# Optimization experiments

Measured on AMD Instinct MI355X. Metric: run time of the kernel, lower is better.

## Reference

```python
import jax, jax.numpy as jnp
import numpy as np


def _sample_choices(prob_weights, key):
    # softmax over edge-type dim, take P(NORMAL_EDGE)=index 1
    prob_edge = jax.nn.softmax(prob_weights, axis=-1)[..., 1]  # [out, in]
    k_bern, k_fix = jax.random.split(key)
    choices = jax.random.bernoulli(k_bern, prob_edge).astype(prob_weights.dtype)  # [out, in]
    # zero-connection fixup: rows with no sampled edge get one random connection
    out_f, in_f = choices.shape
    conn_count = jnp.sum(choices, axis=-1)  # [out]
    rand_cols = jax.random.randint(k_fix, (out_f,), 0, in_f)  # [out]
    fix = ((conn_count == 0)[:, None] & (jnp.arange(in_f)[None, :] == rand_cols[:, None]))
    choices = choices + fix.astype(choices.dtype)
    # selected edges -> 0, unselected -> 1 (min operator branch; no *-1 negation)
    mask = jnp.abs(choices - 1.0)
    return mask


def reference(x, prob_weights):
    # x: [B, in], prob_weights: [out, in, 2]
    mask = _sample_choices(prob_weights, jax.random.key(42))  # [out, in]
    # result[b, o] = min_i (x[b, i] + mask[o, i])  -- [B, out, in] intermediate
    operator_inputs = x[:, None, :] + mask[None, :, :]
    return jnp.min(operator_inputs, axis=-1)  # [B, out]


def setup_inputs() -> dict:
    key = jax.random.key(0)
    k_x, k_w = jax.random.split(key)
    B, IN, OUT = 512, 512, 512
    x = jax.random.uniform(k_x, (B, IN), dtype=jnp.float32)
    prob_weights = jax.random.uniform(k_w, (OUT, IN, 2), dtype=jnp.float32)
    return {"x": x, "prob_weights": prob_weights}
```

## Files before the change

### kernel.cpp

```cpp
#include <hip/hip_runtime.h>
#include <cstdint>

__host__ __device__ inline void threefry2x32(uint32_t k0, uint32_t k1,
                                             uint32_t x0, uint32_t x1,
                                             uint32_t& o0, uint32_t& o1) {
  const uint32_t ks2 = k0 ^ k1 ^ 0x1BD11BDAu;
  uint32_t v0 = x0 + k0, v1 = x1 + k1;
#define RL(v, r) (((v) << (r)) | ((v) >> (32 - (r))))
#define RND4(a, b, c, d)                                                       \
  v0 += v1; v1 = RL(v1, a); v1 ^= v0;                                          \
  v0 += v1; v1 = RL(v1, b); v1 ^= v0;                                          \
  v0 += v1; v1 = RL(v1, c); v1 ^= v0;                                          \
  v0 += v1; v1 = RL(v1, d); v1 ^= v0;
  RND4(13, 15, 26, 6)  v0 += k1;  v1 += ks2 + 1u;
  RND4(17, 29, 16, 24) v0 += ks2; v1 += k0 + 2u;
  RND4(13, 15, 26, 6)  v0 += k0;  v1 += k1 + 3u;
  RND4(17, 29, 16, 24) v0 += k1;  v1 += ks2 + 4u;
  RND4(13, 15, 26, 6)  v0 += ks2; v1 += k0 + 5u;
#undef RND4
#undef RL
  o0 = v0; o1 = v1;
}

#define IN_F 512
#define OUT_F 512
#define BATCH 512

__global__ __launch_bounds__(512) void gen_mask_kernel(
    const float* __restrict__ pw, float* __restrict__ M,
    uint32_t kb0, uint32_t kb1, uint32_t kl0, uint32_t kl1) {
  const int o = blockIdx.x;
  const int i = threadIdx.x;

  const float2 w = ((const float2*)pw)[o * IN_F + i];
  const float mx = fmaxf(w.x, w.y);
  const float e0 = expf(w.x - mx);
  const float e1 = expf(w.y - mx);
  const float p = e1 / (e0 + e1);

  const uint32_t n = (uint32_t)(o * IN_F + i);
  uint32_t h0, h1;
  threefry2x32(kb0, kb1, 0u, n, h0, h1);
  const uint32_t bits = h0 ^ h1;
  const float u = __uint_as_float((bits >> 9) | 0x3F800000u) - 1.0f;
  const bool c = u < p;

  __shared__ unsigned long long words[8];
  __shared__ int cnt;
  if (i == 0) cnt = 0;
  __syncthreads();
  const unsigned long long bal = __ballot(c);
  if ((i & 63) == 0) {
    words[i >> 6] = bal;
    atomicAdd(&cnt, __popcll(bal));
  }
  __syncthreads();
  if (cnt == 0 && i == 0) {
    uint32_t c0, c1;
    threefry2x32(kl0, kl1, 0u, (uint32_t)o, c0, c1);
    const uint32_t rb = c0 ^ c1;
    const uint32_t col = rb & (IN_F - 1);
    words[col >> 6] |= (1ull << (col & 63u));
  }
  __syncthreads();
  const bool sel = (words[i >> 6] >> (i & 63)) & 1ull;
  M[o * IN_F + i] = sel ? 0.0f : 1e9f;
}

#define BT 32
#define OT 16
#define KT 128

__global__ __launch_bounds__(256) void minplus_kernel(
    const float* __restrict__ x, const float* __restrict__ M,
    float* __restrict__ out) {
  __shared__ float xs[KT][BT + 1];
  __shared__ float ms[KT][OT + 1];

  const int tid = threadIdx.x;
  const int tx = tid & 15;
  const int ty = tid >> 4;
  const int b0 = blockIdx.x * BT;
  const int o0 = blockIdx.y * OT;

  const int sr = tid >> 5;
  const int sc = (tid & 31) * 4;

  float acc0 = 1e30f, acc1 = 1e30f;

  for (int kt = 0; kt < IN_F; kt += KT) {
#pragma unroll
    for (int j = 0; j < 4; ++j) {
      const int r = j * 8 + sr;
      const float4 v = *(const float4*)&x[(b0 + r) * IN_F + kt + sc];
      xs[sc + 0][r] = v.x; xs[sc + 1][r] = v.y;
      xs[sc + 2][r] = v.z; xs[sc + 3][r] = v.w;
    }
#pragma unroll
    for (int j = 0; j < 2; ++j) {
      const int r = j * 8 + sr;
      const float4 v = *(const float4*)&M[(o0 + r) * IN_F + kt + sc];
      ms[sc + 0][r] = v.x; ms[sc + 1][r] = v.y;
      ms[sc + 2][r] = v.z; ms[sc + 3][r] = v.w;
    }
    __syncthreads();
#pragma unroll 16
    for (int k = 0; k < KT; ++k) {
      const float2 xv = *(const float2*)&xs[k][tx * 2];
      const float mv = ms[k][ty];
      acc0 = fminf(acc0, xv.x + mv);
      acc1 = fminf(acc1, xv.y + mv);
    }
    __syncthreads();
  }

  out[(b0 + tx * 2 + 0) * OUT_F + o0 + ty] = acc0;
  out[(b0 + tx * 2 + 1) * OUT_F + o0 + ty] = acc1;
}

extern "C" void kernel_launch(void* const* d_in, const int* in_sizes, int n_in,
                              void* d_out, int out_size, void* d_ws, size_t ws_size,
                              hipStream_t stream) {
  (void)in_sizes; (void)n_in; (void)out_size; (void)ws_size;
  const float* x = (const float*)d_in[0];
  const float* pw = (const float*)d_in[1];
  float* M = (float*)d_ws;
  float* out = (float*)d_out;

  uint32_t kb0, kb1, kf0, kf1, kl0, kl1;
  threefry2x32(0u, 42u, 0u, 0u, kb0, kb1);
  threefry2x32(0u, 42u, 0u, 1u, kf0, kf1);
  threefry2x32(kf0, kf1, 0u, 1u, kl0, kl1);

  gen_mask_kernel<<<dim3(OUT_F), dim3(IN_F), 0, stream>>>(pw, M, kb0, kb1, kl0, kl1);
  minplus_kernel<<<dim3(BATCH / BT, OUT_F / OT), dim3(256), 0, stream>>>(x, M, out);
}
```

Baseline: 75.57 us.

## Restructure min-plus kernel with async LDS double-buffered mask and wave-uniform x loads

Rewrites the min-plus kernel so each lane owns one output column and each wave handles four batch rows. x rows are read from global memory with wave-uniform (broadcast) float4 loads. Mask tiles are staged into LDS with async global_load_lds into a double buffer, using an XOR swizzle to avoid bank conflicts. This aims to cut LDS transpose stores and synchronisation overhead and to overlap mask loads with compute. The tradeoffs are fewer blocks (32x8) and reliance on cached x reads.

```diff
diff --git a/kernel.cpp b/kernel.cpp
--- a/kernel.cpp
+++ b/kernel.cpp
@@ -67,55 +67,80 @@
   M[o * IN_F + i] = sel ? 0.0f : 1e9f;
 }
 
-#define BT 32
-#define OT 16
-#define KT 128
+#define OTILE 64
+#define KT2 128
+#define NB 4
 
-__global__ __launch_bounds__(256) void minplus_kernel(
+__global__ __launch_bounds__(256) void minplus2_kernel(
     const float* __restrict__ x, const float* __restrict__ M,
     float* __restrict__ out) {
-  __shared__ float xs[KT][BT + 1];
-  __shared__ float ms[KT][OT + 1];
+  __shared__ float ms[2][OTILE * KT2];
 
   const int tid = threadIdx.x;
-  const int tx = tid & 15;
-  const int ty = tid >> 4;
-  const int b0 = blockIdx.x * BT;
-  const int o0 = blockIdx.y * OT;
+  const int lane = tid & 63;
+  const int w = __builtin_amdgcn_readfirstlane(tid >> 6);
+  const int o0 = blockIdx.y * OTILE;
+  const int bb = blockIdx.x * (4 * NB) + w * NB;
 
-  const int sr = tid >> 5;
-  const int sc = (tid & 31) * 4;
+  const int swz = (lane & 7) << 4;
 
-  float acc0 = 1e30f, acc1 = 1e30f;
+  auto stage = [&](int c, int s) {
+    const int lr = lane >> 5;
+    const int q = (lane & 31) << 4;
+#pragma unroll
+    for (int j = 0; j < 8; ++j) {
+      const int r = w * 16 + 2 * j + lr;
+      const float* src = M + (size_t)(o0 + r) * IN_F + c * KT2 +
+                         ((q ^ ((r & 7) << 4)) >> 2);
+      __builtin_amdgcn_global_load_lds(
+          (const __attribute__((address_space(1))) void*)src,
+          (__attribute__((address_space(3))) void*)&ms[s][(w * 16 + 2 * j) * KT2],
+          16, 0, 0);
+    }
+  };
 
-  for (int kt = 0; kt < IN_F; kt += KT) {
-#pragma unroll
-    for (int j = 0; j < 4; ++j) {
-      const int r = j * 8 + sr;
-      const float4 v = *(const float4*)&x[(b0 + r) * IN_F + kt + sc];
-      xs[sc + 0][r] = v.x; xs[sc + 1][r] = v.y;
-      xs[sc + 2][r] = v.z; xs[sc + 3][r] = v.w;
-    }
-#pragma unroll
-    for (int j = 0; j < 2; ++j) {
-      const int r = j * 8 + sr;
-      const float4 v = *(const float4*)&M[(o0 + r) * IN_F + kt + sc];
-      ms[sc + 0][r] = v.x; ms[sc + 1][r] = v.y;
-      ms[sc + 2][r] = v.z; ms[sc + 3][r] = v.w;
-    }
-    __syncthreads();
-#pragma unroll 16
-    for (int k = 0; k < KT; ++k) {
-      const float2 xv = *(const float2*)&xs[k][tx * 2];
-      const float mv = ms[k][ty];
-      acc0 = fminf(acc0, xv.x + mv);
-      acc1 = fminf(acc1, xv.y + mv);
+  float acc0 = 1e30f, acc1 = 1e30f, acc2 = 1e30f, acc3 = 1e30f;
+
+  stage(0, 0);
+  __syncthreads();
+
+  for (int c = 0; c < IN_F / KT2; ++c) {
+    if (c + 1 < IN_F / KT2) stage(c + 1, (c + 1) & 1);
+
+    const char* mrow = (const char*)&ms[c & 1][0] + lane * (KT2 * 4);
+    const float* xb = x + c * KT2;
+
+#pragma unroll 8
+    for (int k4 = 0; k4 < KT2; k4 += 4) {
+      const float4 mv = *(const float4*)(mrow + ((k4 * 4) ^ swz));
+      {
+        const float4 xv = *(const float4*)&xb[(bb + 0) * IN_F + k4];
+        acc0 = fminf(acc0, fminf(fminf(xv.x + mv.x, xv.y + mv.y),
+                                 fminf(xv.z + mv.z, xv.w + mv.w)));
+      }
+      {
+        const float4 xv = *(const float4*)&xb[(bb + 1) * IN_F + k4];
+        acc1 = fminf(acc1, fminf(fminf(xv.x + mv.x, xv.y + mv.y),
+                                 fminf(xv.z + mv.z, xv.w + mv.w)));
+      }
+      {
+        const float4 xv = *(const float4*)&xb[(bb + 2) * IN_F + k4];
+        acc2 = fminf(acc2, fminf(fminf(xv.x + mv.x, xv.y + mv.y),
+                                 fminf(xv.z + mv.z, xv.w + mv.w)));
+      }
+      {
+        const float4 xv = *(const float4*)&xb[(bb + 3) * IN_F + k4];
+        acc3 = fminf(acc3, fminf(fminf(xv.x + mv.x, xv.y + mv.y),
+                                 fminf(xv.z + mv.z, xv.w + mv.w)));
+      }
     }
     __syncthreads();
   }
 
-  out[(b0 + tx * 2 + 0) * OUT_F + o0 + ty] = acc0;
-  out[(b0 + tx * 2 + 1) * OUT_F + o0 + ty] = acc1;
+  out[(size_t)(bb + 0) * OUT_F + o0 + lane] = acc0;
+  out[(size_t)(bb + 1) * OUT_F + o0 + lane] = acc1;
+  out[(size_t)(bb + 2) * OUT_F + o0 + lane] = acc2;
+  out[(size_t)(bb + 3) * OUT_F + o0 + lane] = acc3;
 }
 
 extern "C" void kernel_launch(void* const* d_in, const int* in_sizes, int n_in,
@@ -133,5 +158,5 @@
   threefry2x32(kf0, kf1, 0u, 1u, kl0, kl1);
 
   gen_mask_kernel<<<dim3(OUT_F), dim3(IN_F), 0, stream>>>(pw, M, kb0, kb1, kl0, kl1);
-  minplus_kernel<<<dim3(BATCH / BT, OUT_F / OT), dim3(256), 0, stream>>>(x, M, out);
+  minplus2_kernel<<<dim3(BATCH / (4 * NB), OUT_F / OTILE), dim3(256), 0, stream>>>(x, M, out);
 }
```

After: 76.05 us. Within noise of the previous version (+0.6%).
